# Performance work log

Measured on AMD Instinct MI355X. Metric: run time of the kernel, lower is better.

## Reference

```python
import jax, jax.numpy as jnp
import numpy as np

B, T, V, E, H = 16, 32, 1003, 100, 2048


def setup_inputs() -> dict:
    key = jax.random.key(0)
    ks = jax.random.split(key, 16)
    s = 0.02
    n = lambda k, shape: (jax.random.normal(k, shape, jnp.float32) * s)
    tokens = jax.random.randint(ks[0], (B, T), 0, V, dtype=jnp.int32)
    return {
        "tokens": tokens,
        "emb": n(ks[1], (V, E)),
        "W1": n(ks[2], (E, 4 * H)), "U1": n(ks[3], (H, 4 * H)), "b1": jnp.zeros((4 * H,), jnp.float32),
        "W2": n(ks[4], (H, 4 * H)), "U2": n(ks[5], (H, 4 * H)), "b2": jnp.zeros((4 * H,), jnp.float32),
        "W3": n(ks[6], (H, 4 * H)), "U3": n(ks[7], (H, 4 * H)), "b3": jnp.zeros((4 * H,), jnp.float32),
        "Wd1": n(ks[8], (H, H)), "bd1": jnp.zeros((H,), jnp.float32),
        "Wd2": n(ks[9], (H, V)), "bd2": jnp.zeros((V,), jnp.float32),
    }


def masked_lstm(x, mask, W, U, b):
    """Keras-semantics masked LSTM. x: [B,T,D], mask: [B,T] bool.
    Masked steps carry h,c through unchanged (cuDNN-incompatible path).
    Returns (all_h: [B,T,H], last_h: [B,H])."""
    Hd = U.shape[0]
    Bd = x.shape[0]
    # precompute input projections for all timesteps at once: [T,B,4H]
    xz = jnp.einsum('btd,dh->tbh', x, W) + b
    m_t = jnp.swapaxes(mask, 0, 1)  # [T,B]

    def step(carry, inp):
        h, c = carry
        zx, mt = inp
        z = zx + h @ U  # [B,4H]
        i, f, g, o = jnp.split(z, 4, axis=-1)
        i = jax.nn.sigmoid(i)
        f = jax.nn.sigmoid(f)
        g = jnp.tanh(g)
        o = jax.nn.sigmoid(o)
        c_new = f * c + i * g
        h_new = o * jnp.tanh(c_new)
        m = mt[:, None]
        h_new = jnp.where(m, h_new, h)
        c_new = jnp.where(m, c_new, c)
        return (h_new, c_new), h_new

    init = (jnp.zeros((Bd, Hd), x.dtype), jnp.zeros((Bd, Hd), x.dtype))
    (h_last, _), hs = jax.lax.scan(step, init, (xz, m_t))
    return jnp.swapaxes(hs, 0, 1), h_last


def reference(tokens, emb, W1, U1, b1, W2, U2, b2, W3, U3, b3, Wd1, bd1, Wd2, bd2):
    mask = tokens != 0  # mask_zero=True semantics
    x = emb[tokens]  # [B,T,E]
    x, _ = masked_lstm(x, mask, W1, U1, b1)
    x, _ = masked_lstm(x, mask, W2, U2, b2)
    _, h = masked_lstm(x, mask, W3, U3, b3)  # return_sequences=False -> last (carried) state
    y = h @ Wd1 + bd1  # Dense, linear activation
    logits = y @ Wd2 + bd2
    return jax.nn.softmax(logits, axis=-1)
```

## Files before the change

### kernel.cpp

```cpp
#include <hip/hip_runtime.h>
#include <hip/hip_bf16.h>
#include <cstddef>

#define BB 16
#define TT 32
#define VV 1003
#define EE 100
#define HH 2048
#define G4 8192

typedef __attribute__((ext_vector_type(4))) float f32x4;
typedef unsigned char u8;

#define SA 64.0f
#define SB 128.0f
#define DESCALE 1.220703125e-4f

__device__ __forceinline__ unsigned pk_lo(unsigned old, float a, float b) {
  return (unsigned)__builtin_amdgcn_cvt_pk_fp8_f32(a, b, (int)old, false);
}
__device__ __forceinline__ unsigned pk_hi(unsigned old, float a, float b) {
  return (unsigned)__builtin_amdgcn_cvt_pk_fp8_f32(a, b, (int)old, true);
}
__device__ __forceinline__ u8 cvt1fp8(float a) {
  return (u8)(__builtin_amdgcn_cvt_pk_fp8_f32(a, 0.f, 0, false) & 0xff);
}
__device__ __forceinline__ long mklong(unsigned lo, unsigned hi) {
  return (long)(((unsigned long long)hi << 32) | lo);
}

__global__ __launch_bounds__(256) void embed_frag(
    const int* __restrict__ tokens, const float* __restrict__ emb,
    u8* __restrict__ xf) {
  int i = blockIdx.x * 256 + threadIdx.x;
  if (i >= TT * BB * 128) return;
  int e = i & 127, b = (i >> 7) & 15, t = i >> 11;
  float v = 0.f;
  if (e < EE) v = emb[(size_t)tokens[b * TT + t] * EE + e] * SA;
  int kt = e >> 5, kk = e & 31;
  int lane = (kk >> 3) * 16 + b, j = kk & 7;
  xf[(size_t)t * 2048 + (size_t)(kt >> 1) * 1024 + lane * 16 + (kt & 1) * 8 + j] =
      cvt1fp8(v);
}

__device__ __forceinline__ void split_body(
    u8* __restrict__ ldb,
    const float* __restrict__ src, u8* __restrict__ dst,
    int Kreal, int nkt2, int pair, int ct0, int tid) {
  int r0 = pair * 64;
#pragma unroll
  for (int p = 0; p < 4; p++) {
    int c4 = tid & 63, rq = p * 4 + (tid >> 6);
    int c = c4 * 4;
    int g = c >> 6;
    int rel = c & 63;
    int row = rq * 4;
    float4 v[4];
#pragma unroll
    for (int i = 0; i < 4; i++) {
      int r = r0 + row + i;
      v[i] = (r < Kreal)
          ? *(const float4*)&src[(size_t)r * G4 + (size_t)g * HH + ct0 * 4 + rel]
          : make_float4(0.f, 0.f, 0.f, 0.f);
    }
#pragma unroll
    for (int j = 0; j < 4; j++) {
      unsigned w = 0;
      w = pk_lo(w, ((const float*)&v[0])[j] * SB, ((const float*)&v[1])[j] * SB);
      w = pk_hi(w, ((const float*)&v[2])[j] * SB, ((const float*)&v[3])[j] * SB);
      int cc = c + j;
      *(unsigned*)&ldb[cc * 72 + g * 8 + row] = w;
    }
  }
  __syncthreads();
  int L = tid & 63;
  int cl = L & 15, g = cl >> 2, hq = cl & 3;
  int row0 = (L >> 4) * 8;
#pragma unroll
  for (int pass = 0; pass < 4; pass++) {
    int ctr = (tid >> 6) + pass * 4;
    int cc = g * 64 + ctr * 4 + hq;
    const u8* bp = &ldb[cc * 72 + g * 8];
    uint2 h0 = *(const uint2*)&bp[row0];
    uint2 h1 = *(const uint2*)&bp[32 + row0];
    *(uint4*)&dst[((size_t)(ct0 + ctr) * nkt2 + pair) * 1024 + L * 16] =
        make_uint4(h0.x, h0.y, h1.x, h1.y);
  }
}

__global__ __launch_bounds__(256, 8) void split_wu(
    const float* __restrict__ srcW, u8* __restrict__ dstW, int KrealW, int nkt2W,
    const float* __restrict__ srcU, u8* __restrict__ dstU) {
  __shared__ __align__(16) u8 ldb[256 * 72 + 16];
  int tid = threadIdx.x;
  int bx = blockIdx.x, ct0 = blockIdx.y * 16;
  if (bx < nkt2W)
    split_body(ldb, srcW, dstW, KrealW, nkt2W, bx, ct0, tid);
  else
    split_body(ldb, srcU, dstU, HH, 32, bx - nkt2W, ct0, tid);
}

__global__ __launch_bounds__(512) void gemm_mfma(
    const u8* __restrict__ af, int t_stride, int nkt2,
    const u8* __restrict__ wfrag, const float* __restrict__ bias,
    float* __restrict__ xz,
    unsigned* __restrict__ hzero,
    unsigned* __restrict__ hcz) {
  __shared__ __align__(16) u8 Bs[3][8][1024];
  int tid = threadIdx.x;
  int w = tid >> 6, L = tid & 63;
  int ct0 = blockIdx.x * 8;
  int t_a = blockIdx.y * 4 + (w & 3);
  int nt0 = (w >> 2) * 4;

  if (blockIdx.y == 0) {
    if (tid < 128) hzero[blockIdx.x * 128 + tid] = 0u;
    hcz[blockIdx.x * 1024 + tid] = 0u;
    hcz[blockIdx.x * 1024 + 512 + tid] = 0u;
  }

  f32x4 acc[4];
#pragma unroll
  for (int i = 0; i < 4; i++) acc[i] = (f32x4){0.f, 0.f, 0.f, 0.f};
  const u8* Ah = af + (size_t)t_a * t_stride + L * 16;

  int s_nt = tid >> 6, boff = (tid & 63) * 16;

  {
    uint4 t0 = *(const uint4*)&wfrag[((size_t)(ct0 + s_nt) * nkt2 + 0) * 1024 + boff];
    *(uint4*)&Bs[0][s_nt][boff] = t0;
    if (nkt2 > 1) {
      uint4 t1 = *(const uint4*)&wfrag[((size_t)(ct0 + s_nt) * nkt2 + 1) * 1024 + boff];
      *(uint4*)&Bs[1][s_nt][boff] = t1;
    }
  }
  __syncthreads();

  for (int s = 0; s < nkt2; s++) {
    uint4 nx;
    bool pf = (s + 2 < nkt2);
    if (pf)
      nx = *(const uint4*)&wfrag[((size_t)(ct0 + s_nt) * nkt2 + s + 2) * 1024 + boff];
    int buf = s % 3;
    uint4 a = *(const uint4*)(Ah + (size_t)s * 1024);
    long a0 = mklong(a.x, a.y), a1 = mklong(a.z, a.w);
#pragma unroll
    for (int i = 0; i < 4; i++) {
      uint4 bb = *(const uint4*)&Bs[buf][nt0 + i][L * 16];
      acc[i] = __builtin_amdgcn_mfma_f32_16x16x32_fp8_fp8(a0, mklong(bb.x, bb.y), acc[i], 0, 0, 0);
      acc[i] = __builtin_amdgcn_mfma_f32_16x16x32_fp8_fp8(a1, mklong(bb.z, bb.w), acc[i], 0, 0, 0);
    }
    if (pf) *(uint4*)&Bs[(s + 2) % 3][s_nt][boff] = nx;
    __syncthreads();
  }

  int nq = L >> 4, hl = L & 15;
#pragma unroll
  for (int i = 0; i < 4; i++) {
    int ctg = ct0 + nt0 + i;
    int gcol = (hl >> 2) * HH + ctg * 4 + (hl & 3);
    float bv = bias[gcol];
#pragma unroll
    for (int r = 0; r < 4; r++) {
      int b = nq * 4 + r;
      xz[((size_t)t_a * 16 + b) * G4 + ctg * 16 + hl] = acc[i][r] * DESCALE + bv;
    }
  }
}

__global__ __launch_bounds__(1024, 8) void lstm_step(
    const u8* __restrict__ Ufrag,
    const float* __restrict__ xzt,
    const u8* __restrict__ hf_in,
    u8* __restrict__ hf_out,
    const float* __restrict__ hT_in,
    float* __restrict__ hT_out,
    float* __restrict__ c,
    const int* __restrict__ tokens, int t) {
  __shared__ float red[16][16][16];
  __shared__ float zs[16][16];
  int tid = threadIdx.x, w = tid >> 6, L = tid & 63;
  int ct = blockIdx.x;

  float xzv = 0.f;
  if (tid < 256) xzv = xzt[(size_t)(tid >> 4) * G4 + ct * 16 + (tid & 15)];
  float c_old = 0.f, h_old = 0.f;
  int tok = 1;
  if (tid < 64) {
    int b = tid >> 2, hq = tid & 3;
    int hu = ct * 4 + hq;
    c_old = c[(size_t)b * HH + hu];
    h_old = hT_in[(size_t)hu * BB + b];
    tok = tokens[b * TT + t];
  }

  f32x4 acc = {0.f, 0.f, 0.f, 0.f};
  const u8* Ub = Ufrag + ((size_t)ct * 32 + w * 2) * 1024 + L * 16;
  const u8* Hb = hf_in + (size_t)(w * 2) * 1024 + L * 16;

#pragma unroll
  for (int i = 0; i < 2; i++) {
    uint4 u = *(const uint4*)(Ub + i * 1024);
    uint4 h = *(const uint4*)(Hb + i * 1024);
    acc = __builtin_amdgcn_mfma_f32_16x16x32_fp8_fp8(mklong(h.x, h.y), mklong(u.x, u.y), acc, 0, 0, 0);
    acc = __builtin_amdgcn_mfma_f32_16x16x32_fp8_fp8(mklong(h.z, h.w), mklong(u.z, u.w), acc, 0, 0, 0);
  }
#pragma unroll
  for (int r = 0; r < 4; r++) red[w][(L >> 4) * 4 + r][L & 15] = acc[r];
  __syncthreads();

  if (tid < 256) {
    int b = tid >> 4, cl = tid & 15;
    float s = 0.f;
#pragma unroll
    for (int q = 0; q < 16; q++) s += red[q][b][cl];
    zs[b][cl] = s * DESCALE + xzv;
  }
  __syncthreads();

  if (tid < 64) {
    int b = tid >> 2, hq = tid & 3;
    int hu = ct * 4 + hq;
    float z0 = zs[b][0 + hq];
    float z1 = zs[b][4 + hq];
    float z2 = zs[b][8 + hq];
    float z3 = zs[b][12 + hq];
    float ig = 1.f / (1.f + expf(-z0));
    float fg = 1.f / (1.f + expf(-z1));
    float gt = tanhf(z2);
    float og = 1.f / (1.f + expf(-z3));
    float cn = fg * c_old + ig * gt;
    float hn = og * tanhf(cn);
    if (tok == 0) {
      cn = c_old;
      hn = h_old;
    }
    c[(size_t)b * HH + hu] = cn;
    hT_out[(size_t)hu * BB + b] = hn;
    int kt2 = hu >> 5, kk = hu & 31;
    int lane2 = (kk >> 3) * 16 + b, jj = kk & 7;
    hf_out[(size_t)(kt2 >> 1) * 1024 + lane2 * 16 + (kt2 & 1) * 8 + jj] =
        cvt1fp8(hn * SA);
  }
}

__global__ __launch_bounds__(256) void head_partial(
    const float* __restrict__ XT, const float* __restrict__ W,
    float* __restrict__ partial, int N) {
  __shared__ float xs[2048];
  int tid = threadIdx.x;
  int k0 = blockIdx.y * 128;
  const float* src = XT + (size_t)k0 * 16;
  for (int i = tid; i < 2048; i += 256) xs[i] = src[i];
  __syncthreads();
  int kg = tid >> 6, lane = tid & 63;
  int col = blockIdx.x * 64 + lane;
  if (col >= N) return;
  float acc[16];
#pragma unroll
  for (int b = 0; b < 16; b++) acc[b] = 0.f;
  const float* Wp = W + (size_t)(k0 + kg * 32) * N + col;
  const float* xp = xs + kg * 32 * 16;
  for (int kk = 0; kk < 32; kk++) {
    float wv = Wp[(size_t)kk * N];
#pragma unroll
    for (int b = 0; b < 16; b++) acc[b] = fmaf(xp[kk * 16 + b], wv, acc[b]);
  }
  int chunk = blockIdx.y * 4 + kg;
#pragma unroll
  for (int b = 0; b < 16; b++)
    partial[((size_t)chunk * 16 + b) * N + col] = acc[b];
}

__global__ __launch_bounds__(256) void head_reduce(
    const float* __restrict__ partial, const float* __restrict__ bias,
    float* __restrict__ out, int N, int sc, int sb) {
  int i = blockIdx.x * 256 + threadIdx.x;
  if (i >= 16 * N) return;
  int b = i / N, col = i - b * N;
  float s = bias[col];
#pragma unroll 8
  for (int ch = 0; ch < 64; ch++) s += partial[((size_t)ch * 16 + b) * N + col];
  out[(size_t)col * sc + (size_t)b * sb] = s;
}

__global__ __launch_bounds__(256) void softmax_rows(
    const float* __restrict__ logits, float* __restrict__ out, int N) {
  __shared__ float buf[1024];
  __shared__ float wred[4];
  __shared__ float rmax, rsum;
  int b = blockIdx.x, tid = threadIdx.x;
  float m = -1e30f;
  for (int v = tid; v < N; v += 256) {
    float x = logits[(size_t)b * N + v];
    buf[v] = x;
    m = fmaxf(m, x);
  }
  for (int o = 32; o > 0; o >>= 1) m = fmaxf(m, __shfl_down(m, o, 64));
  if ((tid & 63) == 0) wred[tid >> 6] = m;
  __syncthreads();
  if (tid == 0) rmax = fmaxf(fmaxf(wred[0], wred[1]), fmaxf(wred[2], wred[3]));
  __syncthreads();
  float s = 0.f;
  for (int v = tid; v < N; v += 256) {
    float e = expf(buf[v] - rmax);
    buf[v] = e;
    s += e;
  }
  for (int o = 32; o > 0; o >>= 1) s += __shfl_down(s, o, 64);
  if ((tid & 63) == 0) wred[tid >> 6] = s;
  __syncthreads();
  if (tid == 0) rsum = wred[0] + wred[1] + wred[2] + wred[3];
  __syncthreads();
  float inv = 1.f / rsum;
  for (int v = tid; v < N; v += 256) out[(size_t)b * N + v] = buf[v] * inv;
}

extern "C" void kernel_launch(void* const* d_in, const int* in_sizes, int n_in,
                              void* d_out, int out_size, void* d_ws, size_t ws_size,
                              hipStream_t stream) {
  const int*   tokens = (const int*)d_in[0];
  const float* emb  = (const float*)d_in[1];
  const float* W1   = (const float*)d_in[2];
  const float* U1   = (const float*)d_in[3];
  const float* b1   = (const float*)d_in[4];
  const float* W2   = (const float*)d_in[5];
  const float* U2   = (const float*)d_in[6];
  const float* b2   = (const float*)d_in[7];
  const float* W3   = (const float*)d_in[8];
  const float* U3   = (const float*)d_in[9];
  const float* b3   = (const float*)d_in[10];
  const float* Wd1  = (const float*)d_in[11];
  const float* bd1  = (const float*)d_in[12];
  const float* Wd2  = (const float*)d_in[13];
  const float* bd2  = (const float*)d_in[14];
  float* out = (float*)d_out;

  char* base = (char*)d_ws;
  size_t off = 0;
  auto carve = [&](size_t bytes) -> char* {
    char* p = base + off;
    off += (bytes + 255) & ~(size_t)255;
    return p;
  };
  float* xz      = (float*)carve((size_t)TT * BB * G4 * 4);
  u8*    allhf0  = (u8*)carve(33ull * 32768);
  u8*    allhf1  = (u8*)carve(33ull * 32768);
  u8*    allhf2  = (u8*)carve(33ull * 32768);
  u8*    xfrag   = (u8*)carve((size_t)TT * 2048);
  u8*    wfrag   = (u8*)carve(512ull * 64 * 512);
  u8*    ufrag   = (u8*)carve(512ull * 64 * 512);
  float* hT0     = (float*)carve(2 * HH * BB * 4);
  float* cbuf    = hT0 + HH * BB;
  float* hT1     = (float*)carve(HH * BB * 4);
  float* yT      = (float*)carve(HH * BB * 4);
  float* logits  = (float*)carve(BB * 1024 * 4);
  float* partial = (float*)carve(64ull * 16 * HH * 4);

  u8* allhf[3] = {allhf0, allhf1, allhf2};
  const float* Us[3] = {U1, U2, U3};
  const float* Ws[3] = {W1, W2, W3};
  const float* bs[3] = {b1, b2, b3};
  float* hping[2] = {hT0, hT1};

  embed_frag<<<dim3(256), 256, 0, stream>>>(tokens, emb, xfrag);

  for (int layer = 0; layer < 3; layer++) {
    const u8* af;
    int t_stride, nkt2W, KrealW;
    if (layer == 0) {
      af = xfrag; t_stride = 2048; nkt2W = 2; KrealW = EE;
    } else {
      af = allhf[layer - 1] + 32768;
      t_stride = 32768; nkt2W = 32; KrealW = HH;
    }
    split_wu<<<dim3(nkt2W + 32, 32), 256, 0, stream>>>(
        Ws[layer], wfrag, KrealW, nkt2W, Us[layer], ufrag);
    gemm_mfma<<<dim3(64, 8), 512, 0, stream>>>(
        af, t_stride, nkt2W, wfrag, bs[layer], xz,
        (unsigned*)allhf[layer], (unsigned*)hT0);
    for (int t = 0; t < TT; t++) {
      lstm_step<<<dim3(512), 1024, 0, stream>>>(
          ufrag, xz + (size_t)t * BB * G4,
          allhf[layer] + (size_t)t * 32768, allhf[layer] + (size_t)(t + 1) * 32768,
          hping[t & 1], hping[(t + 1) & 1], cbuf, tokens, t);
    }
  }

  head_partial<<<dim3(HH / 64, 16), 256, 0, stream>>>(hT0, Wd1, partial, HH);
  head_reduce<<<dim3((16 * HH + 255) / 256), 256, 0, stream>>>(partial, bd1, yT, HH, 16, 1);
  head_partial<<<dim3((VV + 63) / 64, 16), 256, 0, stream>>>(yT, Wd2, partial, VV);
  head_reduce<<<dim3((16 * VV + 255) / 256), 256, 0, stream>>>(partial, bd2, logits, VV, 1, VV);
  softmax_rows<<<dim3(BB), 256, 0, stream>>>(logits, out, VV);
}
```

Baseline: 585.9 us.

## Overlap next-layer weight FP8 conversion with LSTM recurrent steps

Next-layer W/U fp32-to-fp8 fragment conversion moves into extra blocks of the per-timestep lstm_step launches, with double-buffered fragment buffers, so it no longer runs as a standalone kernel between layers. Each timestep converts two 64-row units across 32 column tiles. lstm_step also drops from 1024 to 512 threads, each wave now doing four k-chunks instead of two, which halves the shared-memory reduction width. The risk is that the extra blocks lengthen each latency-bound recurrent step, and fewer waves give less parallelism per block.

```diff
diff --git a/kernel.cpp b/kernel.cpp
--- a/kernel.cpp
+++ b/kernel.cpp
@@ -74,13 +74,13 @@
   }
   __syncthreads();
   int L = tid & 63;
-  int cl = L & 15, g = cl >> 2, hq = cl & 3;
+  int cl = L & 15, gg = cl >> 2, hq = cl & 3;
   int row0 = (L >> 4) * 8;
 #pragma unroll
   for (int pass = 0; pass < 4; pass++) {
     int ctr = (tid >> 6) + pass * 4;
-    int cc = g * 64 + ctr * 4 + hq;
-    const u8* bp = &ldb[cc * 72 + g * 8];
+    int cc = gg * 64 + ctr * 4 + hq;
+    const u8* bp = &ldb[cc * 72 + gg * 8];
     uint2 h0 = *(const uint2*)&bp[row0];
     uint2 h1 = *(const uint2*)&bp[32 + row0];
     *(uint4*)&dst[((size_t)(ct0 + ctr) * nkt2 + pair) * 1024 + L * 16] =
@@ -88,7 +88,49 @@
   }
 }
 
-__global__ __launch_bounds__(256, 8) void split_wu(
+__device__ __forceinline__ void split_body_512(
+    u8* __restrict__ ldb,
+    const float* __restrict__ src, u8* __restrict__ dst,
+    int nkt2, int pair, int ct0, int tid) {
+  int r0 = pair * 64;
+  int c4 = tid & 63;
+  int c = c4 * 4;
+  int g = c >> 6;
+  int rel = c & 63;
+  int rg = tid >> 6;
+  const float* colbase = src + (size_t)g * HH + ct0 * 4 + rel;
+  float4 v[8];
+#pragma unroll
+  for (int i = 0; i < 8; i++)
+    v[i] = *(const float4*)&colbase[(size_t)(r0 + rg * 8 + i) * G4];
+#pragma unroll
+  for (int j = 0; j < 4; j++) {
+    unsigned w0 = 0, w1 = 0;
+    w0 = pk_lo(w0, ((const float*)&v[0])[j] * SB, ((const float*)&v[1])[j] * SB);
+    w0 = pk_hi(w0, ((const float*)&v[2])[j] * SB, ((const float*)&v[3])[j] * SB);
+    w1 = pk_lo(w1, ((const float*)&v[4])[j] * SB, ((const float*)&v[5])[j] * SB);
+    w1 = pk_hi(w1, ((const float*)&v[6])[j] * SB, ((const float*)&v[7])[j] * SB);
+    int cc = c + j;
+    *(unsigned*)&ldb[cc * 72 + g * 8 + rg * 8] = w0;
+    *(unsigned*)&ldb[cc * 72 + g * 8 + rg * 8 + 4] = w1;
+  }
+  __syncthreads();
+  int L = tid & 63;
+  int cl = L & 15, gg = cl >> 2, hq = cl & 3;
+  int row0 = (L >> 4) * 8;
+#pragma unroll
+  for (int pass = 0; pass < 2; pass++) {
+    int ctr = (tid >> 6) + pass * 8;
+    int cc = gg * 64 + ctr * 4 + hq;
+    const u8* bp = &ldb[cc * 72 + gg * 8];
+    uint2 h0 = *(const uint2*)&bp[row0];
+    uint2 h1 = *(const uint2*)&bp[32 + row0];
+    *(uint4*)&dst[((size_t)(ct0 + ctr) * nkt2 + pair) * 1024 + L * 16] =
+        make_uint4(h0.x, h0.y, h1.x, h1.y);
+  }
+}
+
+__global__ __launch_bounds__(256) void split_wu(
     const float* __restrict__ srcW, u8* __restrict__ dstW, int KrealW, int nkt2W,
     const float* __restrict__ srcU, u8* __restrict__ dstU) {
   __shared__ __align__(16) u8 ldb[256 * 72 + 16];
@@ -168,7 +210,7 @@
   }
 }
 
-__global__ __launch_bounds__(1024, 8) void lstm_step(
+__global__ __launch_bounds__(512, 8) void lstm_step(
     const u8* __restrict__ Ufrag,
     const float* __restrict__ xzt,
     const u8* __restrict__ hf_in,
@@ -176,10 +218,26 @@
     const float* __restrict__ hT_in,
     float* __restrict__ hT_out,
     float* __restrict__ c,
-    const int* __restrict__ tokens, int t) {
-  __shared__ float red[16][16][16];
-  __shared__ float zs[16][16];
-  int tid = threadIdx.x, w = tid >> 6, L = tid & 63;
+    const int* __restrict__ tokens, int t,
+    const float* __restrict__ srcW, u8* __restrict__ dstW,
+    const float* __restrict__ srcU, u8* __restrict__ dstU) {
+  __shared__ __align__(16) u8 smem[18960];
+  int tid = threadIdx.x;
+
+  if (blockIdx.x >= 512) {
+    int ext = blockIdx.x - 512;
+    int unit = 2 * t + (ext >> 5);
+    int ct0 = (ext & 31) * 16;
+    if (unit < 32)
+      split_body_512(smem, srcW, dstW, 32, unit, ct0, tid);
+    else
+      split_body_512(smem, srcU, dstU, 32, unit - 32, ct0, tid);
+    return;
+  }
+
+  float (*red)[16][16] = (float (*)[16][16])smem;
+  float (*zs)[16] = (float (*)[16])(smem + 8192);
+  int w = tid >> 6, L = tid & 63;
   int ct = blockIdx.x;
 
   float xzv = 0.f;
@@ -195,11 +253,11 @@
   }
 
   f32x4 acc = {0.f, 0.f, 0.f, 0.f};
-  const u8* Ub = Ufrag + ((size_t)ct * 32 + w * 2) * 1024 + L * 16;
-  const u8* Hb = hf_in + (size_t)(w * 2) * 1024 + L * 16;
-
-#pragma unroll
-  for (int i = 0; i < 2; i++) {
+  const u8* Ub = Ufrag + ((size_t)ct * 32 + w * 4) * 1024 + L * 16;
+  const u8* Hb = hf_in + (size_t)(w * 4) * 1024 + L * 16;
+
+#pragma unroll
+  for (int i = 0; i < 4; i++) {
     uint4 u = *(const uint4*)(Ub + i * 1024);
     uint4 h = *(const uint4*)(Hb + i * 1024);
     acc = __builtin_amdgcn_mfma_f32_16x16x32_fp8_fp8(mklong(h.x, h.y), mklong(u.x, u.y), acc, 0, 0, 0);
@@ -213,7 +271,7 @@
     int b = tid >> 4, cl = tid & 15;
     float s = 0.f;
 #pragma unroll
-    for (int q = 0; q < 16; q++) s += red[q][b][cl];
+    for (int q = 0; q < 8; q++) s += red[q][b][cl];
     zs[b][cl] = s * DESCALE + xzv;
   }
   __syncthreads();
@@ -348,8 +406,10 @@
   u8*    allhf1  = (u8*)carve(33ull * 32768);
   u8*    allhf2  = (u8*)carve(33ull * 32768);
   u8*    xfrag   = (u8*)carve((size_t)TT * 2048);
-  u8*    wfrag   = (u8*)carve(512ull * 64 * 512);
-  u8*    ufrag   = (u8*)carve(512ull * 64 * 512);
+  u8*    wf0     = (u8*)carve(512ull * 64 * 512);
+  u8*    uf0     = (u8*)carve(512ull * 64 * 512);
+  u8*    wf1     = (u8*)carve(512ull * 64 * 512);
+  u8*    uf1     = (u8*)carve(512ull * 64 * 512);
   float* hT0     = (float*)carve(2 * HH * BB * 4);
   float* cbuf    = hT0 + HH * BB;
   float* hT1     = (float*)carve(HH * BB * 4);
@@ -362,28 +422,38 @@
   const float* Ws[3] = {W1, W2, W3};
   const float* bs[3] = {b1, b2, b3};
   float* hping[2] = {hT0, hT1};
+  u8* wfl[3] = {wf0, wf1, wf0};
+  u8* ufl[3] = {uf0, uf1, uf0};
 
   embed_frag<<<dim3(256), 256, 0, stream>>>(tokens, emb, xfrag);
+
+  split_wu<<<dim3(2 + 32, 32), 256, 0, stream>>>(Ws[0], wf0, EE, 2, Us[0], uf0);
 
   for (int layer = 0; layer < 3; layer++) {
     const u8* af;
-    int t_stride, nkt2W, KrealW;
+    int t_stride, nkt2W;
     if (layer == 0) {
-      af = xfrag; t_stride = 2048; nkt2W = 2; KrealW = EE;
+      af = xfrag; t_stride = 2048; nkt2W = 2;
     } else {
       af = allhf[layer - 1] + 32768;
-      t_stride = 32768; nkt2W = 32; KrealW = HH;
-    }
-    split_wu<<<dim3(nkt2W + 32, 32), 256, 0, stream>>>(
-        Ws[layer], wfrag, KrealW, nkt2W, Us[layer], ufrag);
+      t_stride = 32768; nkt2W = 32;
+    }
     gemm_mfma<<<dim3(64, 8), 512, 0, stream>>>(
-        af, t_stride, nkt2W, wfrag, bs[layer], xz,
+        af, t_stride, nkt2W, wfl[layer], bs[layer], xz,
         (unsigned*)allhf[layer], (unsigned*)hT0);
+
+    bool hide = (layer < 2);
+    int grid = hide ? 576 : 512;
+    const float* sW = hide ? Ws[layer + 1] : Ws[layer];
+    u8* dW = wfl[layer + 1 == 3 ? 0 : layer + 1];
+    const float* sU = hide ? Us[layer + 1] : Us[layer];
+    u8* dU = ufl[layer + 1 == 3 ? 0 : layer + 1];
     for (int t = 0; t < TT; t++) {
-      lstm_step<<<dim3(512), 1024, 0, stream>>>(
-          ufrag, xz + (size_t)t * BB * G4,
+      lstm_step<<<dim3(grid), 512, 0, stream>>>(
+          ufl[layer], xz + (size_t)t * BB * G4,
           allhf[layer] + (size_t)t * 32768, allhf[layer] + (size_t)(t + 1) * 32768,
-          hping[t & 1], hping[(t + 1) & 1], cbuf, tokens, t);
+          hping[t & 1], hping[(t + 1) & 1], cbuf, tokens, t,
+          sW, dW, sU, dU);
     }
   }
 
```

Result: slower. 603.1 us (+2.9%).
